# Kernel tuning notes

Hardware: AMD Instinct MI355X
Metric: run time of the kernel (lower is better)

Reference implementation:

```python
import math
import jax, jax.numpy as jnp
import numpy as np

B, QDIM, KDIM, EMBED, HEADS, H, W = 2, 192, 192, 256, 8, 48, 48


def setup_inputs() -> dict:
    key = jax.random.key(0)
    ks = jax.random.split(key, 8)
    s = 0.05
    return {
        "query": jax.random.normal(ks[0], (B, QDIM, H, W), dtype=jnp.float32),
        "key": jax.random.normal(ks[1], (B, KDIM, H, W), dtype=jnp.float32),
        "Wq": jax.random.normal(ks[2], (EMBED, QDIM), dtype=jnp.float32) * s,
        "bq": jax.random.normal(ks[3], (EMBED,), dtype=jnp.float32) * s,
        "Wk": jax.random.normal(ks[4], (EMBED, KDIM), dtype=jnp.float32) * s,
        "bk": jax.random.normal(ks[5], (EMBED,), dtype=jnp.float32) * s,
        "Wv": jax.random.normal(ks[6], (EMBED, KDIM), dtype=jnp.float32) * s,
        "bv": jax.random.normal(ks[7], (EMBED,), dtype=jnp.float32) * s,
        "num_heads": HEADS,
    }


def reference(query, key, Wq, bq, Wk, bk, Wv, bv, num_heads):
    b, qdim, h, w = query.shape
    L = h * w
    embed = Wq.shape[0]
    hd = embed // num_heads

    # (B, C, H, W) -> (B, L, C) raster order
    q = query.transpose(0, 2, 3, 1).reshape(b, L, qdim)
    k_in = key.transpose(0, 2, 3, 1).reshape(b, L, -1)

    q = q @ Wq.T + bq               # (B, L, E)
    v = k_in @ Wv.T + bv            # (B, L, E)
    k = k_in @ Wk.T + bk            # (B, L, E)

    q = q.reshape(b, L, num_heads, hd).transpose(0, 2, 1, 3)  # bhqd
    k = k.reshape(b, L, num_heads, hd).transpose(0, 2, 1, 3)  # bhkd
    v = v.reshape(b, L, num_heads, hd).transpose(0, 2, 1, 3)  # bhkd

    scores = jnp.einsum("bhqd,bhkd->bhqk", q, k) / math.sqrt(hd)
    # causal (square subsequent) mask: -inf strictly above diagonal
    idx = jnp.arange(L)
    neg = jnp.asarray(jnp.finfo(scores.dtype).min, scores.dtype)
    mask = jnp.where(idx[:, None] >= idx[None, :], jnp.zeros((), scores.dtype), neg)
    scores = scores + mask

    attn = jax.nn.softmax(scores, axis=-1)  # dropout p=0.0 (eval)
    x = jnp.einsum("bhqk,bhkd->bhqd", attn, v)  # (B, H, L, hd)

    # (B, H, L, hd) -> (B, H, hd, L) -> (B, E, h, w)
    out = x.transpose(0, 1, 3, 2).reshape(b, embed, h, w)
    return out
```

## Files before the change

kernel.cpp:

```cpp
#include <hip/hip_runtime.h>

#define LQ 2304
#define CIN 192
#define EMB 256
#define NH 8
#define HD 32

typedef __attribute__((ext_vector_type(8))) short short8;
typedef __attribute__((ext_vector_type(4))) short short4v;
typedef __attribute__((ext_vector_type(4))) float floatx4;
typedef __attribute__((ext_vector_type(16))) float f32x16;

__device__ __forceinline__ unsigned short f2bf(float f) {
  union { float f; unsigned u; } v; v.f = f;
  unsigned r = v.u + 0x7FFFu + ((v.u >> 16) & 1u);
  return (unsigned short)(r >> 16);
}
__device__ __forceinline__ unsigned cvtpk(float lo, float hi) {
  unsigned r;
  asm("v_cvt_pk_bf16_f32 %0, %1, %2" : "=v"(r) : "v"(lo), "v"(hi));
  return r;
}
__device__ __forceinline__ void plswap(unsigned& a, unsigned& b, int hi) {
#if __has_builtin(__builtin_amdgcn_permlane32_swap)
  auto r = __builtin_amdgcn_permlane32_swap((int)a, (int)b, false, false);
  a = (unsigned)r[0]; b = (unsigned)r[1];
#else
  unsigned pa = (unsigned)__shfl_xor((int)a, 32);
  unsigned pb = (unsigned)__shfl_xor((int)b, 32);
  unsigned na = hi ? pb : a;
  unsigned nb = hi ? b : pa;
  a = na; b = nb;
#endif
}
__device__ __forceinline__ float xmax(float x, int hi) {
  unsigned a = __float_as_uint(x), b = a;
  plswap(a, b, hi);
  return fmaxf(__uint_as_float(a), __uint_as_float(b));
}
__device__ __forceinline__ float xadd(float x, int hi) {
  unsigned a = __float_as_uint(x), b = a;
  plswap(a, b, hi);
  return __uint_as_float(a) + __uint_as_float(b);
}

__global__ __launch_bounds__(256) void k_qkv(
    const float* __restrict__ query, const float* __restrict__ key,
    const float* __restrict__ Wq, const float* __restrict__ Wk, const float* __restrict__ Wv,
    const float* __restrict__ bq, const float* __restrict__ bk, const float* __restrict__ bv,
    unsigned short* Qb, unsigned short* Kb, unsigned short* Vt) {
  __shared__ float tile[64][65];
  __shared__ unsigned short Xs[64][200];

  int proj = blockIdx.z;
  int b = blockIdx.y;
  int l0 = blockIdx.x * 64;
  const float* src  = (proj == 0) ? query : key;
  const float* Wf   = (proj == 0) ? Wq : (proj == 1 ? Wk : Wv);
  const float* bias = (proj == 0) ? bq : (proj == 1 ? bk : bv);
  const float alpha = (proj == 0) ? 0.25505653582177047f : 1.0f;

  int tid = threadIdx.x;
  int j = tid & 63, i0 = tid >> 6;
  const float* sp = src + (size_t)b * CIN * LQ;

  for (int ch = 0; ch < 3; ++ch) {
    int c0 = ch * 64;
    #pragma unroll
    for (int i = i0; i < 64; i += 4)
      tile[i][j] = sp[(size_t)(c0 + i) * LQ + l0 + j];
    __syncthreads();
    #pragma unroll
    for (int li = i0; li < 64; li += 4)
      Xs[li][c0 + j] = f2bf(tile[j][li]);
    __syncthreads();
  }

  int lane = tid & 63, w = tid >> 6;
  int g = lane >> 4, r16 = lane & 15;
  int e0 = w * 64;

  floatx4 acc[4][4];
  #pragma unroll
  for (int a = 0; a < 4; ++a)
    #pragma unroll
    for (int ls = 0; ls < 4; ++ls) acc[a][ls] = (floatx4){0.f, 0.f, 0.f, 0.f};

  #pragma unroll
  for (int ks = 0; ks < CIN; ks += 32) {
    short8 wf[4];
    #pragma unroll
    for (int a = 0; a < 4; ++a) {
      const float* wp = Wf + (size_t)(e0 + a * 16 + r16) * CIN + ks + g * 8;
      union { unsigned u[4]; short8 s; } pk;
      pk.u[0] = cvtpk(wp[0], wp[1]);
      pk.u[1] = cvtpk(wp[2], wp[3]);
      pk.u[2] = cvtpk(wp[4], wp[5]);
      pk.u[3] = cvtpk(wp[6], wp[7]);
      wf[a] = pk.s;
    }
    #pragma unroll
    for (int ls = 0; ls < 4; ++ls) {
      short8 xf = *(const short8*)&Xs[ls * 16 + r16][ks + g * 8];
      #pragma unroll
      for (int a = 0; a < 4; ++a)
        acc[a][ls] = __builtin_amdgcn_mfma_f32_16x16x32_bf16(wf[a], xf, acc[a][ls], 0, 0, 0);
    }
  }

  #pragma unroll
  for (int a = 0; a < 4; ++a) {
    int ebase = e0 + a * 16 + g * 4;
    int h = ebase >> 5, d0 = ebase & 31;
    #pragma unroll
    for (int ls = 0; ls < 4; ++ls) {
      int lg = l0 + ls * 16 + r16;
      if (proj < 2) {
        unsigned short* outp = (proj == 0) ? Qb : Kb;
        short4v pk;
        #pragma unroll
        for (int r = 0; r < 4; ++r)
          pk[r] = (short)f2bf((acc[a][ls][r] + bias[ebase + r]) * alpha);
        *(short4v*)(outp + ((size_t)(b * NH + h) * LQ + lg) * HD + d0) = pk;
      } else {
        #pragma unroll
        for (int r = 0; r < 4; ++r)
          Vt[((size_t)(b * NH + h) * HD + d0 + r) * LQ + lg] =
              f2bf(acc[a][ls][r] + bias[ebase + r]);
      }
    }
  }
}

__device__ __forceinline__ void softmax_pv(f32x16& c0, f32x16& c1, f32x16& O,
                                           float& m, float& sum,
                                           const short8* vf, int hi) {
  float mx;
  {
    float a0 = fmaxf(fmaxf(c0[0], c0[8]),  fmaxf(c1[0], c1[8]));
    float a1 = fmaxf(fmaxf(c0[1], c0[9]),  fmaxf(c1[1], c1[9]));
    float a2 = fmaxf(fmaxf(c0[2], c0[10]), fmaxf(c1[2], c1[10]));
    float a3 = fmaxf(fmaxf(c0[3], c0[11]), fmaxf(c1[3], c1[11]));
    float a4 = fmaxf(fmaxf(c0[4], c0[12]), fmaxf(c1[4], c1[12]));
    float a5 = fmaxf(fmaxf(c0[5], c0[13]), fmaxf(c1[5], c1[13]));
    float a6 = fmaxf(fmaxf(c0[6], c0[14]), fmaxf(c1[6], c1[14]));
    float a7 = fmaxf(fmaxf(c0[7], c0[15]), fmaxf(c1[7], c1[15]));
    mx = fmaxf(fmaxf(fmaxf(a0, a1), fmaxf(a2, a3)),
               fmaxf(fmaxf(a4, a5), fmaxf(a6, a7)));
  }
  mx = xmax(mx, hi);

  if (!__all(mx - m <= 8.0f)) {
    float mn = fmaxf(m, mx);
    float al = exp2f(m - mn);
    sum *= al;
    #pragma unroll
    for (int i = 0; i < 16; ++i) O[i] *= al;
    m = mn;
  }

  #pragma unroll
  for (int i = 0; i < 16; ++i) {
    c0[i] = exp2f(c0[i] - m);
    c1[i] = exp2f(c1[i] - m);
  }
  {
    float a0 = (c0[0] + c0[8])  + (c1[0] + c1[8]);
    float a1 = (c0[1] + c0[9])  + (c1[1] + c1[9]);
    float a2 = (c0[2] + c0[10]) + (c1[2] + c1[10]);
    float a3 = (c0[3] + c0[11]) + (c1[3] + c1[11]);
    float a4 = (c0[4] + c0[12]) + (c1[4] + c1[12]);
    float a5 = (c0[5] + c0[13]) + (c1[5] + c1[13]);
    float a6 = (c0[6] + c0[14]) + (c1[6] + c1[14]);
    float a7 = (c0[7] + c0[15]) + (c1[7] + c1[15]);
    float ts = ((a0 + a1) + (a2 + a3)) + ((a4 + a5) + (a6 + a7));
    sum += xadd(ts, hi);
  }

  union { unsigned u[4]; short8 s; } pA, pB, pC, pD;
  {
    unsigned a = cvtpk(c0[0], c0[1]), b = cvtpk(c0[2], c0[3]);
    unsigned c = cvtpk(c0[4], c0[5]), d = cvtpk(c0[6], c0[7]);
    plswap(a, c, hi); plswap(b, d, hi);
    pA.u[0] = a; pA.u[1] = b; pA.u[2] = c; pA.u[3] = d;
  }
  {
    unsigned a = cvtpk(c0[8], c0[9]),  b = cvtpk(c0[10], c0[11]);
    unsigned c = cvtpk(c0[12], c0[13]), d = cvtpk(c0[14], c0[15]);
    plswap(a, c, hi); plswap(b, d, hi);
    pB.u[0] = a; pB.u[1] = b; pB.u[2] = c; pB.u[3] = d;
  }
  {
    unsigned a = cvtpk(c1[0], c1[1]), b = cvtpk(c1[2], c1[3]);
    unsigned c = cvtpk(c1[4], c1[5]), d = cvtpk(c1[6], c1[7]);
    plswap(a, c, hi); plswap(b, d, hi);
    pC.u[0] = a; pC.u[1] = b; pC.u[2] = c; pC.u[3] = d;
  }
  {
    unsigned a = cvtpk(c1[8], c1[9]),  b = cvtpk(c1[10], c1[11]);
    unsigned c = cvtpk(c1[12], c1[13]), d = cvtpk(c1[14], c1[15]);
    plswap(a, c, hi); plswap(b, d, hi);
    pD.u[0] = a; pD.u[1] = b; pD.u[2] = c; pD.u[3] = d;
  }

  __builtin_amdgcn_s_setprio(1);
  O = __builtin_amdgcn_mfma_f32_32x32x16_bf16(vf[0], pA.s, O, 0, 0, 0);
  O = __builtin_amdgcn_mfma_f32_32x32x16_bf16(vf[1], pB.s, O, 0, 0, 0);
  O = __builtin_amdgcn_mfma_f32_32x32x16_bf16(vf[2], pC.s, O, 0, 0, 0);
  O = __builtin_amdgcn_mfma_f32_32x32x16_bf16(vf[3], pD.s, O, 0, 0, 0);
  __builtin_amdgcn_s_setprio(0);
}

__global__ __launch_bounds__(256, 4) void k_attn(const unsigned short* __restrict__ Qb,
                                                 const unsigned short* __restrict__ Kb,
                                                 const unsigned short* __restrict__ Vt,
                                                 float* __restrict__ out) {
  __shared__ float Osh[4][32][33];
  __shared__ float Msh[4][32];
  __shared__ float Ssh[4][32];

  int bid = blockIdx.x;
  int xcd = bid & 7;
  int idx = bid >> 3;
  int half = idx / 72;
  int j = 71 - (idx - half * 72);
  int bh = xcd + 8 * half;
  int q0b = j * 32;

  int w = threadIdx.x >> 6, lane = threadIdx.x & 63;
  int qcol = lane & 31, hi = lane >> 5;
  int qg = q0b + qcol;

  const unsigned short* Qrow = Qb + ((size_t)bh * LQ + qg) * HD + hi * 8;
  short8 qf0 = *(const short8*)(Qrow);
  short8 qf1 = *(const short8*)(Qrow + 16);

  const f32x16 Z16 = {0,0,0,0,0,0,0,0,0,0,0,0,0,0,0,0};
  f32x16 O = Z16;
  float m = -1e30f, sum = 0.f;

  const unsigned short* Kbase = Kb + (size_t)bh * LQ * HD;
  const unsigned short* Vbase = Vt + (size_t)bh * HD * LQ;
  int ntiles = (q0b + 95) >> 6;

  for (int t = w; t < ntiles; t += 4) {
    int k0 = t * 64;

    short8 kf[4], vf[4];
    {
      const unsigned short* kr = Kbase + (size_t)(k0 + qcol) * HD + hi * 8;
      kf[0] = *(const short8*)(kr);
      kf[1] = *(const short8*)(kr + 16);
      kf[2] = *(const short8*)(kr + 32 * HD);
      kf[3] = *(const short8*)(kr + 32 * HD + 16);
      const unsigned short* vr = Vbase + (size_t)qcol * LQ + k0 + hi * 8;
      vf[0] = *(const short8*)(vr);
      vf[1] = *(const short8*)(vr + 16);
      vf[2] = *(const short8*)(vr + 32);
      vf[3] = *(const short8*)(vr + 48);
    }

    __builtin_amdgcn_s_setprio(1);
    f32x16 c0 = __builtin_amdgcn_mfma_f32_32x32x16_bf16(kf[0], qf0, Z16, 0, 0, 0);
    c0 = __builtin_amdgcn_mfma_f32_32x32x16_bf16(kf[1], qf1, c0, 0, 0, 0);
    f32x16 c1 = __builtin_amdgcn_mfma_f32_32x32x16_bf16(kf[2], qf0, Z16, 0, 0, 0);
    c1 = __builtin_amdgcn_mfma_f32_32x32x16_bf16(kf[3], qf1, c1, 0, 0, 0);
    __builtin_amdgcn_s_setprio(0);

    if (t == ntiles - 1) {
      #pragma unroll
      for (int i = 0; i < 16; ++i) {
        int kg = k0 + (i & 3) + 8 * (i >> 2) + 4 * hi;
        if (kg > qg)      c0[i] = -1e30f;
        if (kg + 32 > qg) c1[i] = -1e30f;
      }
    }

    softmax_pv(c0, c1, O, m, sum, vf, hi);
  }

  #pragma unroll
  for (int i = 0; i < 16; ++i) {
    int d = (i & 3) + 8 * (i >> 2) + 4 * hi;
    Osh[w][d][qcol] = O[i];
  }
  if (hi == 0) { Msh[w][qcol] = m; Ssh[w][qcol] = sum; }
  __syncthreads();

  int tid = threadIdx.x;
  int q = tid & 31, dblk = tid >> 5;
  float m0 = Msh[0][q], m1 = Msh[1][q], m2 = Msh[2][q], m3 = Msh[3][q];
  float ms = fmaxf(fmaxf(m0, m1), fmaxf(m2, m3));
  float a0 = exp2f(m0 - ms), a1 = exp2f(m1 - ms);
  float a2 = exp2f(m2 - ms), a3 = exp2f(m3 - ms);
  float ss = a0 * Ssh[0][q] + a1 * Ssh[1][q] + a2 * Ssh[2][q] + a3 * Ssh[3][q];
  float inv = 1.0f / ss;
  #pragma unroll
  for (int r = 0; r < 4; ++r) {
    int d = dblk * 4 + r;
    float o = a0 * Osh[0][d][q] + a1 * Osh[1][d][q] +
              a2 * Osh[2][d][q] + a3 * Osh[3][d][q];
    out[((size_t)bh * HD + d) * LQ + q0b + q] = o * inv;
  }
}

extern "C" void kernel_launch(void* const* d_in, const int* in_sizes, int n_in,
                              void* d_out, int out_size, void* d_ws, size_t ws_size,
                              hipStream_t stream) {
  const float* query = (const float*)d_in[0];
  const float* key   = (const float*)d_in[1];
  const float* Wq    = (const float*)d_in[2];
  const float* bq    = (const float*)d_in[3];
  const float* Wk    = (const float*)d_in[4];
  const float* bk    = (const float*)d_in[5];
  const float* Wv    = (const float*)d_in[6];
  const float* bv    = (const float*)d_in[7];
  float* out = (float*)d_out;

  unsigned short* Qb = (unsigned short*)d_ws;
  unsigned short* Kb = Qb + 2 * NH * LQ * HD;
  unsigned short* Vt = Kb + 2 * NH * LQ * HD;

  hipLaunchKernelGGL(k_qkv, dim3(36, 2, 3), dim3(256), 0, stream,
                     query, key, Wq, Wk, Wv, bq, bk, bv, Qb, Kb, Vt);
  hipLaunchKernelGGL(k_attn, dim3(1152), dim3(256), 0, stream,
                     Qb, Kb, Vt, out);
}
```

Measured before the change: 46.04 us.

## Prefetch next K tile in attention loop and halve QKV projection tile

```diff
diff --git a/kernel.cpp b/kernel.cpp
--- a/kernel.cpp
+++ b/kernel.cpp
@@ -49,30 +49,31 @@
     const float* __restrict__ Wq, const float* __restrict__ Wk, const float* __restrict__ Wv,
     const float* __restrict__ bq, const float* __restrict__ bk, const float* __restrict__ bv,
     unsigned short* Qb, unsigned short* Kb, unsigned short* Vt) {
-  __shared__ float tile[64][65];
-  __shared__ unsigned short Xs[64][200];
+  __shared__ float tile[64][33];
+  __shared__ unsigned short Xs[32][200];
 
   int proj = blockIdx.z;
   int b = blockIdx.y;
-  int l0 = blockIdx.x * 64;
+  int l0 = blockIdx.x * 32;
   const float* src  = (proj == 0) ? query : key;
   const float* Wf   = (proj == 0) ? Wq : (proj == 1 ? Wk : Wv);
   const float* bias = (proj == 0) ? bq : (proj == 1 ? bk : bv);
   const float alpha = (proj == 0) ? 0.25505653582177047f : 1.0f;
 
   int tid = threadIdx.x;
-  int j = tid & 63, i0 = tid >> 6;
   const float* sp = src + (size_t)b * CIN * LQ;
 
+  int jl = tid & 31, ic0 = tid >> 5;
+  int cc = tid & 63, li0 = tid >> 6;
   for (int ch = 0; ch < 3; ++ch) {
     int c0 = ch * 64;
     #pragma unroll
-    for (int i = i0; i < 64; i += 4)
-      tile[i][j] = sp[(size_t)(c0 + i) * LQ + l0 + j];
+    for (int i = ic0; i < 64; i += 8)
+      tile[i][jl] = sp[(size_t)(c0 + i) * LQ + l0 + jl];
     __syncthreads();
     #pragma unroll
-    for (int li = i0; li < 64; li += 4)
-      Xs[li][c0 + j] = f2bf(tile[j][li]);
+    for (int li = li0; li < 32; li += 4)
+      Xs[li][c0 + cc] = f2bf(tile[cc][li]);
     __syncthreads();
   }
 
@@ -80,11 +81,11 @@
   int g = lane >> 4, r16 = lane & 15;
   int e0 = w * 64;
 
-  floatx4 acc[4][4];
+  floatx4 acc[4][2];
   #pragma unroll
   for (int a = 0; a < 4; ++a)
     #pragma unroll
-    for (int ls = 0; ls < 4; ++ls) acc[a][ls] = (floatx4){0.f, 0.f, 0.f, 0.f};
+    for (int ls = 0; ls < 2; ++ls) acc[a][ls] = (floatx4){0.f, 0.f, 0.f, 0.f};
 
   #pragma unroll
   for (int ks = 0; ks < CIN; ks += 32) {
@@ -100,7 +101,7 @@
       wf[a] = pk.s;
     }
     #pragma unroll
-    for (int ls = 0; ls < 4; ++ls) {
+    for (int ls = 0; ls < 2; ++ls) {
       short8 xf = *(const short8*)&Xs[ls * 16 + r16][ks + g * 8];
       #pragma unroll
       for (int a = 0; a < 4; ++a)
@@ -113,7 +114,7 @@
     int ebase = e0 + a * 16 + g * 4;
     int h = ebase >> 5, d0 = ebase & 31;
     #pragma unroll
-    for (int ls = 0; ls < 4; ++ls) {
+    for (int ls = 0; ls < 2; ++ls) {
       int lg = l0 + ls * 16 + r16;
       if (proj < 2) {
         unsigned short* outp = (proj == 0) ? Qb : Kb;
@@ -243,21 +244,36 @@
   const unsigned short* Vbase = Vt + (size_t)bh * HD * LQ;
   int ntiles = (q0b + 95) >> 6;
 
-  for (int t = w; t < ntiles; t += 4) {
+  int t = w;
+  short8 kf[4];
+  if (t < ntiles) {
+    const unsigned short* kr = Kbase + (size_t)(t * 64 + qcol) * HD + hi * 8;
+    kf[0] = *(const short8*)(kr);
+    kf[1] = *(const short8*)(kr + 16);
+    kf[2] = *(const short8*)(kr + 32 * HD);
+    kf[3] = *(const short8*)(kr + 32 * HD + 16);
+  }
+
+  while (t < ntiles) {
     int k0 = t * 64;
-
-    short8 kf[4], vf[4];
+    int tn = t + 4;
+    int kpre = ((tn < ntiles) ? tn : t) * 64;
+
+    short8 vf[4];
     {
-      const unsigned short* kr = Kbase + (size_t)(k0 + qcol) * HD + hi * 8;
-      kf[0] = *(const short8*)(kr);
-      kf[1] = *(const short8*)(kr + 16);
-      kf[2] = *(const short8*)(kr + 32 * HD);
-      kf[3] = *(const short8*)(kr + 32 * HD + 16);
       const unsigned short* vr = Vbase + (size_t)qcol * LQ + k0 + hi * 8;
       vf[0] = *(const short8*)(vr);
       vf[1] = *(const short8*)(vr + 16);
       vf[2] = *(const short8*)(vr + 32);
       vf[3] = *(const short8*)(vr + 48);
+    }
+    short8 kn[4];
+    {
+      const unsigned short* kr = Kbase + (size_t)(kpre + qcol) * HD + hi * 8;
+      kn[0] = *(const short8*)(kr);
+      kn[1] = *(const short8*)(kr + 16);
+      kn[2] = *(const short8*)(kr + 32 * HD);
+      kn[3] = *(const short8*)(kr + 32 * HD + 16);
     }
 
     __builtin_amdgcn_s_setprio(1);
@@ -277,6 +293,9 @@
     }
 
     softmax_pv(c0, c1, O, m, sum, vf, hi);
+
+    kf[0] = kn[0]; kf[1] = kn[1]; kf[2] = kn[2]; kf[3] = kn[3];
+    t = tn;
   }
 
   #pragma unroll
@@ -321,7 +340,7 @@
   unsigned short* Kb = Qb + 2 * NH * LQ * HD;
   unsigned short* Vt = Kb + 2 * NH * LQ * HD;
 
-  hipLaunchKernelGGL(k_qkv, dim3(36, 2, 3), dim3(256), 0, stream,
+  hipLaunchKernelGGL(k_qkv, dim3(72, 2, 3), dim3(256), 0, stream,
                      query, key, Wq, Wk, Wv, bq, bk, bv, Qb, Kb, Vt);
   hipLaunchKernelGGL(k_attn, dim3(1152), dim3(256), 0, stream,
                      Qb, Kb, Vt, out);
```

Result: slower. 48.82 us (+6.1%).
